# Kernel tuning notes

Hardware: AMD Instinct MI355X
Metric: run time of the kernel (lower is better)

Reference implementation:

```python
import jax, jax.numpy as jnp
import numpy as np

SOS_TOKEN = 0


def setup_inputs() -> dict:
    key = jax.random.key(0)
    ks = jax.random.split(key, 16)
    B, S, T, H, V = 64, 64, 32, 512, 32000
    s = 1.0 / np.sqrt(H)
    inp = {
        "encoder_outputs": jax.random.normal(ks[0], (B, S, H), jnp.float32),
        "encoder_hidden": jax.random.normal(ks[1], (1, B, H), jnp.float32),
        "target_tensor": jax.random.randint(ks[2], (B, T), 0, V),
        "emb": jax.random.normal(ks[3], (V, H), jnp.float32),
        "Wa": jax.random.uniform(ks[4], (H, H), jnp.float32, -s, s),
        "ba": jnp.zeros((H,), jnp.float32),
        "Ua": jax.random.uniform(ks[5], (H, H), jnp.float32, -s, s),
        "bu": jnp.zeros((H,), jnp.float32),
        "va": jax.random.uniform(ks[6], (H, 1), jnp.float32, -s, s),
        "bv": jnp.zeros((1,), jnp.float32),
        "w_ih": jax.random.uniform(ks[7], (3 * H, 2 * H), jnp.float32, -s, s),
        "b_ih": jax.random.uniform(ks[8], (3 * H,), jnp.float32, -s, s),
        "w_hh": jax.random.uniform(ks[9], (3 * H, H), jnp.float32, -s, s),
        "b_hh": jax.random.uniform(ks[10], (3 * H,), jnp.float32, -s, s),
        "Wo": jax.random.uniform(ks[11], (V, H), jnp.float32, -s, s),
        "bo": jax.random.uniform(ks[12], (V,), jnp.float32, -s, s),
    }
    return inp


def _gru_cell(x, h, w_ih, b_ih, w_hh, b_hh):
    # x: [B, 2H], h: [B, H] -- PyTorch nn.GRU gate math
    H = h.shape[-1]
    gi = x @ w_ih.T + b_ih            # [B, 3H]
    gh = h @ w_hh.T + b_hh            # [B, 3H]
    i_r, i_z, i_n = gi[:, :H], gi[:, H:2 * H], gi[:, 2 * H:]
    h_r, h_z, h_n = gh[:, :H], gh[:, H:2 * H], gh[:, 2 * H:]
    r = jax.nn.sigmoid(i_r + h_r)
    z = jax.nn.sigmoid(i_z + h_z)
    n = jnp.tanh(i_n + r * h_n)
    return (1.0 - z) * n + z * h


def reference(encoder_outputs, encoder_hidden, target_tensor,
              emb, Wa, ba, Ua, bu, va, bv,
              w_ih, b_ih, w_hh, b_hh, Wo, bo):
    B, S, H = encoder_outputs.shape
    T = target_tensor.shape[1]
    # Teacher forcing: step t input is SOS for t=0 else target[:, t-1]
    sos = jnp.full((B, 1), SOS_TOKEN, dtype=target_tensor.dtype)
    input_ids = jnp.concatenate([sos, target_tensor[:, :-1]], axis=1)  # [B, T]
    embedded = emb[input_ids]  # [B, T, H]  (dropout is identity in eval)

    # Precompute key projection once (invariant across steps)
    Ua_keys = encoder_outputs @ Ua.T + bu  # [B, S, H]

    def step(h, x_emb):
        # Bahdanau additive attention: query = hidden state
        scores = jnp.tanh(h[:, None, :] @ Wa.T + ba + Ua_keys) @ va + bv  # [B, S, 1]
        scores = scores[..., 0]                                           # [B, S]
        attn = jax.nn.softmax(scores, axis=-1)
        context = jnp.einsum('bs,bsh->bh', attn, encoder_outputs)
        x = jnp.concatenate([x_emb, context], axis=-1)                    # [B, 2H]
        h_new = _gru_cell(x, h, w_ih, b_ih, w_hh, b_hh)
        logits = h_new @ Wo.T + bo                                        # [B, V]
        return h_new, (logits, attn)

    h0 = encoder_hidden[0]  # [B, H]
    h_final, (logits_t, attn_t) = jax.lax.scan(step, h0, jnp.swapaxes(embedded, 0, 1))
    logits = jnp.swapaxes(logits_t, 0, 1)        # [B, T, V]
    attentions = jnp.swapaxes(attn_t, 0, 1)      # [B, T, S]
    log_probs = jax.nn.log_softmax(logits, axis=-1)
    decoder_hidden = h_final[None]               # [1, B, H]
    return (log_probs, decoder_hidden, attentions)
```

## Files before the change

### kernel.cpp

```cpp
#include <hip/hip_runtime.h>

typedef unsigned short u16;
typedef __bf16 bf16x8 __attribute__((ext_vector_type(8)));
typedef float f32x4 __attribute__((ext_vector_type(4)));

#define Bsz 64
#define Ssz 64
#define Tsz 32
#define Hsz 512
#define Vsz 32000
#define NCONV 160
#define NTOT 256

static __device__ inline u16 f2bf(float f) {
    union { float f; unsigned u; } v; v.f = f;
    unsigned u = v.u;
    unsigned r = (u + 0x7FFFu + ((u >> 16) & 1u)) >> 16;
    return (u16)r;
}
static __device__ inline float bf2f(u16 v) {
    union { unsigned u; float f; } x; x.u = ((unsigned)v) << 16; return x.f;
}
static __device__ inline float tanh_fast(float x) {
    float e = __expf(2.f * x);
    return 1.f - 2.f / (e + 1.f);
}
static __device__ inline void st_u32(unsigned* p, unsigned v) {
    __hip_atomic_store(p, v, __ATOMIC_RELAXED, __HIP_MEMORY_SCOPE_AGENT);
}
static __device__ inline unsigned ld_u32(const unsigned* p) {
    return __hip_atomic_load(p, __ATOMIC_RELAXED, __HIP_MEMORY_SCOPE_AGENT);
}

#define GLOAD_LDS16(g, l) \
    __builtin_amdgcn_global_load_lds((const __attribute__((address_space(1))) void*)(g), \
                                     (__attribute__((address_space(3))) void*)(l), 16, 0, 0)

__global__ void prep_kernel(const float* __restrict__ enc, const float* __restrict__ Ua,
                            const float* __restrict__ Wa, const float* __restrict__ wih,
                            const float* __restrict__ whh, const float* __restrict__ ehid,
                            u16* __restrict__ encbf, u16* __restrict__ Uabf,
                            u16* __restrict__ Wabf, u16* __restrict__ wihbf,
                            u16* __restrict__ whhbf, u16* __restrict__ h0bf) {
    const int n0 = 2097152, n1 = 262144, n2 = 262144, n3 = 1572864, n4 = 786432, n5 = 32768;
    const int total = n0 + n1 + n2 + n3 + n4 + n5;
    for (int i = blockIdx.x * blockDim.x + threadIdx.x; i < total; i += gridDim.x * blockDim.x) {
        int j = i;
        if (j < n0) { encbf[j] = f2bf(enc[j]); continue; } j -= n0;
        if (j < n1) { Uabf[j] = f2bf(Ua[j]); continue; } j -= n1;
        if (j < n2) { Wabf[j] = f2bf(Wa[j]); continue; } j -= n2;
        if (j < n3) { wihbf[j] = f2bf(wih[j]); continue; } j -= n3;
        if (j < n4) { whhbf[j] = f2bf(whh[j]); continue; } j -= n4;
        h0bf[j] = f2bf(ehid[j]);
    }
}

__global__ void embed_kernel(const int* __restrict__ target, const float* __restrict__ emb,
                             u16* __restrict__ xbuf) {
    int n = Tsz * Bsz * Hsz;
    for (int i = blockIdx.x * blockDim.x + threadIdx.x; i < n; i += gridDim.x * blockDim.x) {
        int t = i / (Bsz * Hsz);
        int rem = i % (Bsz * Hsz);
        int b = rem / Hsz, k = rem % Hsz;
        int id = (t == 0) ? 0 : target[b * Tsz + (t - 1)];
        xbuf[((size_t)t * Bsz + b) * 1024 + k] = f2bf(emb[(size_t)id * Hsz + k]);
    }
}

__global__ __launch_bounds__(256) void gemm_bt(const u16* __restrict__ A, const u16* __restrict__ Bw,
                                               const float* __restrict__ bias, float* __restrict__ out,
                                               int M, int N, int K) {
    __shared__ __align__(16) u16 As[128 * 32];
    __shared__ __align__(16) u16 Bs[128 * 32];
    int m0 = blockIdx.x * 128, n0 = blockIdx.y * 128;
    int tid = threadIdx.x, lane = tid & 63, wid = tid >> 6;
    int wm = wid & 1, wn = wid >> 1;
    f32x4 acc[4][4] = {};
    for (int k0 = 0; k0 < K; k0 += 32) {
        int e0 = wid * 64 + lane;
        int e1 = e0 + 256;
        GLOAD_LDS16(&A[(size_t)(m0 + (e0 >> 2)) * K + k0 + (e0 & 3) * 8], (char*)As + wid * 1024);
        GLOAD_LDS16(&A[(size_t)(m0 + (e1 >> 2)) * K + k0 + (e1 & 3) * 8], (char*)As + 4096 + wid * 1024);
        GLOAD_LDS16(&Bw[(size_t)(n0 + (e0 >> 2)) * K + k0 + (e0 & 3) * 8], (char*)Bs + wid * 1024);
        GLOAD_LDS16(&Bw[(size_t)(n0 + (e1 >> 2)) * K + k0 + (e1 & 3) * 8], (char*)Bs + 4096 + wid * 1024);
        __syncthreads();
        bf16x8 av[4], bvv[4];
        for (int mi = 0; mi < 4; ++mi)
            av[mi] = *(const bf16x8*)&As[(wm * 64 + mi * 16 + (lane & 15)) * 32 + (lane >> 4) * 8];
        for (int ni = 0; ni < 4; ++ni)
            bvv[ni] = *(const bf16x8*)&Bs[(wn * 64 + ni * 16 + (lane & 15)) * 32 + (lane >> 4) * 8];
        for (int mi = 0; mi < 4; ++mi)
            for (int ni = 0; ni < 4; ++ni)
                acc[mi][ni] = __builtin_amdgcn_mfma_f32_16x16x32_bf16(av[mi], bvv[ni], acc[mi][ni], 0, 0, 0);
        __syncthreads();
    }
    for (int mi = 0; mi < 4; ++mi)
        for (int ni = 0; ni < 4; ++ni) {
            int n = n0 + wn * 64 + ni * 16 + (lane & 15);
            float bb = bias[n];
            for (int r = 0; r < 4; ++r) {
                int m = m0 + wm * 64 + mi * 16 + (lane >> 4) * 4 + r;
                out[(size_t)m * N + n] = acc[mi][ni][r] + bb;
            }
        }
}

static __device__ inline void arrive(unsigned* bar, int slot, unsigned val, int tid) {
    asm volatile("s_waitcnt vmcnt(0)" ::: "memory");
    __syncthreads();
    if (tid == 0) st_u32(&bar[slot * 32], val);
}
static __device__ inline void pollflags(unsigned* bar, int base, int n, unsigned target, int tid) {
    if (tid < n) {
        unsigned* p = &bar[(base + tid) * 32];
        while (ld_u32(p) < target) {}
    }
    __syncthreads();
}

__global__ __launch_bounds__(512, 1) void coop_kernel(
    const float* __restrict__ uak,
    u16* __restrict__ xbuf, u16* __restrict__ Abf,
    const u16* __restrict__ h0bf, const u16* __restrict__ wihbf, const u16* __restrict__ whhbf,
    const u16* __restrict__ Wabf, const float* __restrict__ enc,
    const float* __restrict__ va, const float* __restrict__ bv, const float* __restrict__ ba,
    const float* __restrict__ b_ih, const float* __restrict__ b_hh,
    const float* __restrict__ ehid,
    const float* __restrict__ Wo, u16* __restrict__ Wobf,
    float* __restrict__ out, u16* __restrict__ partials,
    unsigned* __restrict__ bar) {
    __shared__ __align__(16) char lds[149504];
    __shared__ float WhL[512];
    __shared__ float scL[64];
    __shared__ float vaL[512];

    const size_t HID_OFF = (size_t)Bsz * Tsz * Vsz;
    const size_t ATT_OFF = HID_OFF + (size_t)Bsz * Hsz;

    int tid = threadIdx.x, lane = tid & 63, wid = tid >> 6;
    int ln15 = lane & 15, hi = lane >> 4;
    int bx = blockIdx.x;

    unsigned* xbufU = (unsigned*)xbuf;
    unsigned* AbfU = (unsigned*)Abf;
    unsigned* partU = (unsigned*)partials;

    if (bx < 64) {
        int b = bx;
        u16* uakL = (u16*)lds;
        u16* encL = (u16*)(lds + 65536);
        for (int i = tid; i < Ssz * Hsz; i += 512) {
            uakL[i] = f2bf(uak[(size_t)b * Ssz * Hsz + i]);
            encL[i] = f2bf(enc[(size_t)b * Ssz * Hsz + i]);
        }
        vaL[tid] = va[tid];
        float bvv = bv[0];
        float ba_t = ba[tid];
        int halfsel = tid & 1;
        __syncthreads();

        for (int t = 0; t < Tsz; ++t) {
            pollflags(bar, 64, 32, (unsigned)(t + 1), tid);
            {
                float acc = ba_t;
                const unsigned* pb = partU + (size_t)b * 256 + (tid >> 1);
#pragma unroll
                for (int g = 0; g < 32; ++g) {
                    unsigned pw = ld_u32(pb + (size_t)g * 16384);
                    acc += bf2f((u16)(halfsel ? (pw >> 16) : (pw & 0xffff)));
                }
                WhL[tid] = acc;
            }
            __syncthreads();
            for (int si = 0; si < 8; ++si) {
                int s = wid * 8 + si;
                float a = 0.f;
#pragma unroll
                for (int ji = 0; ji < 8; ++ji) {
                    int j = lane + ji * 64;
                    float x = WhL[j] + bf2f(uakL[s * 512 + j]);
                    a += tanh_fast(x) * vaL[j];
                }
                for (int off = 32; off; off >>= 1) a += __shfl_down(a, off);
                if (lane == 0) scL[s] = a + bvv;
            }
            __syncthreads();
            if (wid == 0) {
                float x = scL[lane];
                float mx = x;
                for (int off = 32; off; off >>= 1) mx = fmaxf(mx, __shfl_xor(mx, off));
                float e = __expf(x - mx);
                float sm = e;
                for (int off = 32; off; off >>= 1) sm += __shfl_xor(sm, off);
                float at = e / sm;
                scL[lane] = at;
                out[ATT_OFF + ((size_t)b * Tsz + t) * Ssz + lane] = at;
            }
            __syncthreads();
            float c = 0.f;
            for (int s = 0; s < Ssz; ++s)
                c += scL[s] * bf2f(encL[s * 512 + tid]);
            unsigned me = (unsigned)f2bf(c);
            unsigned other = __shfl_xor(me, 1);
            if ((tid & 1) == 0)
                st_u32(&xbufU[((size_t)t * Bsz + b) * 512 + 256 + (tid >> 1)], me | (other << 16));
            arrive(bar, bx, (unsigned)(t + 1), tid);
        }
    } else if (bx < 96) {
        int g = bx - 64, jbase = g * 16;
        u16* hsl = (u16*)(lds + 147456);
        for (int i = tid; i < 6144; i += 512) {
            int row = i >> 7, c16 = i & 127;
            int Rg = (row >> 4) * 512 + jbase + (row & 15);
            uint4 v = *(const uint4*)&wihbf[(size_t)Rg * 1024 + c16 * 8];
            *(uint4*)(lds + row * 2048 + ((c16 * 16) ^ ((row & 7) << 4))) = v;
        }
        for (int i = tid; i < 3072; i += 512) {
            int row = i >> 6, c16 = i & 63;
            int Rg = (row >> 4) * 512 + jbase + (row & 15);
            uint4 v = *(const uint4*)&whhbf[(size_t)Rg * 512 + c16 * 8];
            *(uint4*)(lds + 98304 + row * 1024 + ((c16 * 16) ^ ((row & 7) << 4))) = v;
        }
        const char* wih_l = lds;
        const char* whh_l = lds + 98304;
        int j = jbase + ln15;
        float bir = b_ih[j] + b_hh[j];
        float biz = b_ih[512 + j] + b_hh[512 + j];
        float bin = b_ih[1024 + j];
        float bhn = b_hh[1024 + j];
        float hp0 = 0.f, hp1 = 0.f, hp2 = 0.f, hp3 = 0.f;
        if (wid < 4) {
            int m = wid;
            hp0 = ehid[(size_t)(m * 16 + hi * 4 + 0) * Hsz + j];
            hp1 = ehid[(size_t)(m * 16 + hi * 4 + 1) * Hsz + j];
            hp2 = ehid[(size_t)(m * 16 + hi * 4 + 2) * Hsz + j];
            hp3 = ehid[(size_t)(m * 16 + hi * 4 + 3) * Hsz + j];
        }
        int swz = (ln15 & 7) << 4;
        bf16x8 zfr = {};
        bf16x8 wfrag[4];
#pragma unroll
        for (int i = 0; i < 4; ++i) {
            int jp = (wid * 4 + i) * 16 + ln15;
            wfrag[i] = (hi < 2) ? *(const bf16x8*)&Wabf[(size_t)jp * 512 + jbase + hi * 8] : zfr;
        }
        for (int i = tid; i < 1024; i += 512)
            hsl[i] = h0bf[(size_t)(i >> 4) * 512 + jbase + (i & 15)];
        __syncthreads();
#pragma unroll
        for (int mt = 0; mt < 4; ++mt) {
            bf16x8 af = (hi < 2) ? *(const bf16x8*)&hsl[(mt * 16 + ln15) * 16 + hi * 8] : zfr;
#pragma unroll
            for (int i = 0; i < 4; ++i) {
                f32x4 pacc = {};
                pacc = __builtin_amdgcn_mfma_f32_16x16x32_bf16(af, wfrag[i], pacc, 0, 0, 0);
                int n0 = (wid * 4 + i) * 16;
#pragma unroll
                for (int r = 0; r < 4; ++r) {
                    int b = mt * 16 + hi * 4 + r;
                    unsigned me = (unsigned)f2bf(pacc[r]);
                    unsigned other = __shfl_xor(me, 1);
                    if ((ln15 & 1) == 0)
                        st_u32(&partU[((size_t)g * 64 + b) * 256 + ((n0 + ln15) >> 1)], me | (other << 16));
                }
            }
        }
        arrive(bar, bx, 1u, tid);

        for (int t = 0; t < Tsz; ++t) {
            const u16* hbt = t ? (Abf + (size_t)(t - 1) * Bsz * Hsz) : h0bf;
            pollflags(bar, 64, 32, (unsigned)(t + 1), tid);
            f32x4 ar = {}, az = {}, ain = {}, ahn = {};
            if (wid < 4) {
                int m = wid;
#pragma unroll 8
                for (int k0 = 0; k0 < 16; ++k0) {
                    bf16x8 a = *(const bf16x8*)&xbuf[((size_t)t * Bsz + m * 16 + ln15) * 1024 + k0 * 32 + hi * 8];
                    int byteIn = k0 * 64 + hi * 16;
                    bf16x8 b0 = *(const bf16x8*)(wih_l + (0 + ln15) * 2048 + (byteIn ^ swz));
                    bf16x8 b1 = *(const bf16x8*)(wih_l + (16 + ln15) * 2048 + (byteIn ^ swz));
                    bf16x8 b2 = *(const bf16x8*)(wih_l + (32 + ln15) * 2048 + (byteIn ^ swz));
                    ar = __builtin_amdgcn_mfma_f32_16x16x32_bf16(a, b0, ar, 0, 0, 0);
                    az = __builtin_amdgcn_mfma_f32_16x16x32_bf16(a, b1, az, 0, 0, 0);
                    ain = __builtin_amdgcn_mfma_f32_16x16x32_bf16(a, b2, ain, 0, 0, 0);
                }
#pragma unroll 8
                for (int k0 = 0; k0 < 16; ++k0) {
                    bf16x8 a = *(const bf16x8*)&hbt[(size_t)(m * 16 + ln15) * 512 + k0 * 32 + hi * 8];
                    int byteIn = k0 * 64 + hi * 16;
                    bf16x8 b0 = *(const bf16x8*)(whh_l + (0 + ln15) * 1024 + (byteIn ^ swz));
                    bf16x8 b1 = *(const bf16x8*)(whh_l + (16 + ln15) * 1024 + (byteIn ^ swz));
                    bf16x8 b2 = *(const bf16x8*)(whh_l + (32 + ln15) * 1024 + (byteIn ^ swz));
                    ar = __builtin_amdgcn_mfma_f32_16x16x32_bf16(a, b0, ar, 0, 0, 0);
                    az = __builtin_amdgcn_mfma_f32_16x16x32_bf16(a, b1, az, 0, 0, 0);
                    ahn = __builtin_amdgcn_mfma_f32_16x16x32_bf16(a, b2, ahn, 0, 0, 0);
                }
                unsigned* p = &bar[(wid * 16 + ln15) * 32];
                while (ld_u32(p) < (unsigned)(t + 1)) {}
#pragma unroll 8
                for (int k0 = 16; k0 < 32; ++k0) {
                    bf16x8 a = *(const bf16x8*)&xbuf[((size_t)t * Bsz + m * 16 + ln15) * 1024 + k0 * 32 + hi * 8];
                    int byteIn = k0 * 64 + hi * 16;
                    bf16x8 b0 = *(const bf16x8*)(wih_l + (0 + ln15) * 2048 + (byteIn ^ swz));
                    bf16x8 b1 = *(const bf16x8*)(wih_l + (16 + ln15) * 2048 + (byteIn ^ swz));
                    bf16x8 b2 = *(const bf16x8*)(wih_l + (32 + ln15) * 2048 + (byteIn ^ swz));
                    ar = __builtin_amdgcn_mfma_f32_16x16x32_bf16(a, b0, ar, 0, 0, 0);
                    az = __builtin_amdgcn_mfma_f32_16x16x32_bf16(a, b1, az, 0, 0, 0);
                    ain = __builtin_amdgcn_mfma_f32_16x16x32_bf16(a, b2, ain, 0, 0, 0);
                }
                float hpv[4] = {hp0, hp1, hp2, hp3};
#pragma unroll
                for (int r = 0; r < 4; ++r) {
                    int b = m * 16 + hi * 4 + r;
                    float rg = 1.f / (1.f + __expf(-(ar[r] + bir)));
                    float zg = 1.f / (1.f + __expf(-(az[r] + biz)));
                    float ng = tanh_fast(ain[r] + bin + rg * (ahn[r] + bhn));
                    float hv = (1.f - zg) * ng + zg * hpv[r];
                    hpv[r] = hv;
                    u16 hb = f2bf(hv);
                    unsigned me = (unsigned)hb;
                    unsigned other = __shfl_xor(me, 1);
                    if ((ln15 & 1) == 0)
                        st_u32(&AbfU[((size_t)t * Bsz + b) * 256 + (j >> 1)], me | (other << 16));
                    hsl[b * 16 + ln15] = hb;
                    if (t == Tsz - 1) out[HID_OFF + (size_t)b * 512 + j] = hv;
                }
                hp0 = hpv[0]; hp1 = hpv[1]; hp2 = hpv[2]; hp3 = hpv[3];
            }
            __syncthreads();
#pragma unroll
            for (int mt = 0; mt < 4; ++mt) {
                bf16x8 af = (hi < 2) ? *(const bf16x8*)&hsl[(mt * 16 + ln15) * 16 + hi * 8] : zfr;
#pragma unroll
                for (int i = 0; i < 4; ++i) {
                    f32x4 pacc = {};
                    pacc = __builtin_amdgcn_mfma_f32_16x16x32_bf16(af, wfrag[i], pacc, 0, 0, 0);
                    int n0 = (wid * 4 + i) * 16;
#pragma unroll
                    for (int r = 0; r < 4; ++r) {
                        int b = mt * 16 + hi * 4 + r;
                        unsigned me = (unsigned)f2bf(pacc[r]);
                        unsigned other = __shfl_xor(me, 1);
                        if ((ln15 & 1) == 0)
                            st_u32(&partU[((size_t)g * 64 + b) * 256 + ((n0 + ln15) >> 1)], me | (other << 16));
                    }
                }
            }
            arrive(bar, bx, (unsigned)(t + 2), tid);
        }
    } else {
        const float4* W4 = (const float4*)Wo;
        for (int i = (bx - 96) * 512 + tid; i < (Vsz * Hsz) / 4; i += NCONV * 512) {
            float4 v = W4[i];
            ushort4 o;
            o.x = f2bf(v.x); o.y = f2bf(v.y); o.z = f2bf(v.z); o.w = f2bf(v.w);
            *(ushort4*)&Wobf[(size_t)i * 4] = o;
        }
    }
}

static __device__ inline void l_stage(const u16* __restrict__ Abf, const u16* __restrict__ Wobf,
                                      int m0, int n0, int k0, char* As, char* Bs, int wid, int lane) {
    int e0 = wid * 64 + lane;
    int r = e0 >> 2, c8 = (e0 & 3) * 8;
    GLOAD_LDS16(&Abf[(size_t)(m0 + r) * 512 + k0 + c8], As + wid * 1024);
    GLOAD_LDS16(&Wobf[(size_t)(n0 + r) * 512 + k0 + c8], Bs + wid * 1024);
    GLOAD_LDS16(&Wobf[(size_t)(n0 + 128 + r) * 512 + k0 + c8], Bs + 8192 + wid * 1024);
}

__global__ __launch_bounds__(512) void gemm_logits(const u16* __restrict__ Abf, const u16* __restrict__ Wobf,
                                                   const float* __restrict__ bo, float* __restrict__ out,
                                                   float* __restrict__ sumexp) {
    __shared__ __align__(16) char lds[49152];
    char* As0 = lds;
    char* Bs0 = lds + 8192;
    char* As1 = lds + 24576;
    char* Bs1 = lds + 32768;
    int tid = threadIdx.x, lane = tid & 63, wid = tid >> 6;
    int ln15 = lane & 15, hi = lane >> 4;
    int wm = wid & 1, wn = wid >> 1;
    int job = blockIdx.x;
    int m0 = (job / 125) * 128, n0 = (job % 125) * 256;
    f32x4 acc[4][4] = {};
    l_stage(Abf, Wobf, m0, n0, 0, As0, Bs0, wid, lane);
#pragma unroll 2
    for (int ks = 0; ks < 16; ++ks) {
        const u16* As = (const u16*)((ks & 1) ? As1 : As0);
        const u16* Bs = (const u16*)((ks & 1) ? Bs1 : Bs0);
        if (ks < 15) {
            l_stage(Abf, Wobf, m0, n0, (ks + 1) * 32,
                    (ks & 1) ? As0 : As1, (ks & 1) ? Bs0 : Bs1, wid, lane);
            asm volatile("s_waitcnt vmcnt(3)" ::: "memory");
        } else {
            asm volatile("s_waitcnt vmcnt(0)" ::: "memory");
        }
        __builtin_amdgcn_s_barrier();
        bf16x8 av[4], bvv[4];
        for (int mi = 0; mi < 4; ++mi)
            av[mi] = *(const bf16x8*)&As[(wm * 64 + mi * 16 + ln15) * 32 + hi * 8];
        for (int ni = 0; ni < 4; ++ni)
            bvv[ni] = *(const bf16x8*)&Bs[(wn * 64 + ni * 16 + ln15) * 32 + hi * 8];
        for (int mi = 0; mi < 4; ++mi)
            for (int ni = 0; ni < 4; ++ni)
                acc[mi][ni] = __builtin_amdgcn_mfma_f32_16x16x32_bf16(av[mi], bvv[ni], acc[mi][ni], 0, 0, 0);
        asm volatile("s_waitcnt lgkmcnt(0)" ::: "memory");
        __builtin_amdgcn_s_barrier();
    }
    float rowpart[4][4];
    for (int mi = 0; mi < 4; ++mi)
        for (int r = 0; r < 4; ++r) rowpart[mi][r] = 0.f;
    for (int mi = 0; mi < 4; ++mi)
        for (int ni = 0; ni < 4; ++ni) {
            int n = n0 + wn * 64 + ni * 16 + ln15;
            float bb = bo[n];
            for (int r = 0; r < 4; ++r) {
                int m = m0 + wm * 64 + mi * 16 + hi * 4 + r;
                int t = m >> 6, b = m & 63;
                float val = acc[mi][ni][r] + bb;
                out[((size_t)(b * Tsz + t)) * Vsz + n] = val;
                rowpart[mi][r] += __expf(val);
            }
        }
    for (int mi = 0; mi < 4; ++mi)
        for (int r = 0; r < 4; ++r) {
            float v = rowpart[mi][r];
            v += __shfl_xor(v, 1);
            v += __shfl_xor(v, 2);
            v += __shfl_xor(v, 4);
            v += __shfl_xor(v, 8);
            if (ln15 == 0) {
                int m = m0 + wm * 64 + mi * 16 + hi * 4 + r;
                atomicAdd(&sumexp[(m & 63) * Tsz + (m >> 6)], v);
            }
        }
}

__global__ void sub_kernel(float* __restrict__ out, const float* __restrict__ sumexp) {
    const int total4 = (Bsz * Tsz * Vsz) / 4;
    float4* o4 = (float4*)out;
    for (int i = blockIdx.x * blockDim.x + threadIdx.x; i < total4; i += gridDim.x * blockDim.x) {
        float l = __logf(sumexp[i / (Vsz / 4)]);
        float4 v = o4[i];
        v.x -= l; v.y -= l; v.z -= l; v.w -= l;
        o4[i] = v;
    }
}

extern "C" void kernel_launch(void* const* d_in, const int* in_sizes, int n_in,
                              void* d_out, int out_size, void* d_ws, size_t ws_size,
                              hipStream_t stream) {
    const float* enc   = (const float*)d_in[0];
    const float* ehid  = (const float*)d_in[1];
    const int*   target= (const int*)d_in[2];
    const float* emb   = (const float*)d_in[3];
    const float* Wa    = (const float*)d_in[4];
    const float* ba    = (const float*)d_in[5];
    const float* Ua    = (const float*)d_in[6];
    const float* bu    = (const float*)d_in[7];
    const float* va    = (const float*)d_in[8];
    const float* bv    = (const float*)d_in[9];
    const float* w_ih  = (const float*)d_in[10];
    const float* b_ih  = (const float*)d_in[11];
    const float* w_hh  = (const float*)d_in[12];
    const float* b_hh  = (const float*)d_in[13];
    const float* Wo    = (const float*)d_in[14];
    const float* bo    = (const float*)d_in[15];
    float* out = (float*)d_out;

    char* w = (char*)d_ws;
    float* uak    = (float*)w; w += (size_t)4096 * 512 * 4;
    float* sumexp = (float*)w; w += 8192;
    unsigned* bar = (unsigned*)w; w += 96 * 128;
    u16* xbuf     = (u16*)w;   w += (size_t)Tsz * Bsz * 1024 * 2;
    u16* Abf      = (u16*)w;   w += (size_t)Tsz * Bsz * Hsz * 2;
    u16* h0bf     = (u16*)w;   w += (size_t)Bsz * Hsz * 2;
    u16* partials = (u16*)w;   w += (size_t)32 * Bsz * Hsz * 2;
    u16* Wabf     = (u16*)w;   w += (size_t)Hsz * Hsz * 2;
    u16* encbf    = (u16*)w;   w += (size_t)4096 * 512 * 2;
    u16* Uabf     = (u16*)w;   w += (size_t)Hsz * Hsz * 2;
    u16* wihbf    = (u16*)w;   w += (size_t)1536 * 1024 * 2;
    u16* whhbf    = (u16*)w;   w += (size_t)1536 * 512 * 2;
    u16* Wobf     = (u16*)w;   w += (size_t)Vsz * 512 * 2;

    prep_kernel<<<2048, 256, 0, stream>>>(enc, Ua, Wa, w_ih, w_hh, ehid,
                                          encbf, Uabf, Wabf, wihbf, whhbf, h0bf);
    embed_kernel<<<1024, 256, 0, stream>>>(target, emb, xbuf);

    gemm_bt<<<dim3(32, 4), 256, 0, stream>>>(encbf, Uabf, bu, uak, 4096, 512, 512);

    hipMemsetAsync(bar, 0, 96 * 128, stream);
    hipMemsetAsync(sumexp, 0, 2048 * 4, stream);

    coop_kernel<<<NTOT, 512, 0, stream>>>(uak, xbuf, Abf, h0bf, wihbf, whhbf,
                                          Wabf, enc, va, bv, ba, b_ih, b_hh,
                                          ehid, Wo, Wobf, out, partials, bar);

    gemm_logits<<<2000, 512, 0, stream>>>(Abf, Wobf, bo, out, sumexp);

    sub_kernel<<<2048, 256, 0, stream>>>(out, sumexp);
}
```

Measured before the change: 976.4 us.

## Fuse logits GEMM into persistent coop kernel, overlapping with recurrent steps

The 160 spare blocks of the persistent kernel, which used to only convert Wo to bf16, now also compute the vocabulary-projection GEMM tiles. Each tile waits on the GRU step flags for the two timesteps it covers, so the logits GEMM runs while later recurrent steps are still executing, and the separate gemm_logits launch is removed. The spin-wait loops also gain s_sleep so polling blocks take fewer issue slots. The costs are extra flag polling, a grid-wide wait on the conversion counter, and competition for memory bandwidth and CUs with the latency-critical recurrent blocks.

```diff
diff --git a/kernel.cpp b/kernel.cpp
--- a/kernel.cpp
+++ b/kernel.cpp
@@ -9,7 +9,7 @@
 #define Tsz 32
 #define Hsz 512
 #define Vsz 32000
-#define NCONV 160
+#define NLBLK 160
 #define NTOT 256
 
 static __device__ inline u16 f2bf(float f) {
@@ -110,10 +110,17 @@
     __syncthreads();
     if (tid == 0) st_u32(&bar[slot * 32], val);
 }
-static __device__ inline void pollflags(unsigned* bar, int base, int n, unsigned target, int tid) {
+static __device__ inline void pollflags1(unsigned* bar, int base, int n, unsigned target, int tid) {
     if (tid < n) {
         unsigned* p = &bar[(base + tid) * 32];
-        while (ld_u32(p) < target) {}
+        while (ld_u32(p) < target) asm volatile("s_sleep 1");
+    }
+    __syncthreads();
+}
+static __device__ inline void pollflags8(unsigned* bar, int base, int n, unsigned target, int tid) {
+    if (tid < n) {
+        unsigned* p = &bar[(base + tid) * 32];
+        while (ld_u32(p) < target) asm volatile("s_sleep 8");
     }
     __syncthreads();
 }
@@ -126,8 +133,8 @@
     const float* __restrict__ va, const float* __restrict__ bv, const float* __restrict__ ba,
     const float* __restrict__ b_ih, const float* __restrict__ b_hh,
     const float* __restrict__ ehid,
-    const float* __restrict__ Wo, u16* __restrict__ Wobf,
-    float* __restrict__ out, u16* __restrict__ partials,
+    const float* __restrict__ Wo, u16* __restrict__ Wobf, const float* __restrict__ bo,
+    float* __restrict__ out, u16* __restrict__ partials, float* __restrict__ sumexp,
     unsigned* __restrict__ bar) {
     __shared__ __align__(16) char lds[149504];
     __shared__ float WhL[512];
@@ -160,7 +167,7 @@
         __syncthreads();
 
         for (int t = 0; t < Tsz; ++t) {
-            pollflags(bar, 64, 32, (unsigned)(t + 1), tid);
+            pollflags1(bar, 64, 32, (unsigned)(t + 1), tid);
             {
                 float acc = ba_t;
                 const unsigned* pb = partU + (size_t)b * 256 + (tid >> 1);
@@ -269,7 +276,7 @@
 
         for (int t = 0; t < Tsz; ++t) {
             const u16* hbt = t ? (Abf + (size_t)(t - 1) * Bsz * Hsz) : h0bf;
-            pollflags(bar, 64, 32, (unsigned)(t + 1), tid);
+            pollflags1(bar, 64, 32, (unsigned)(t + 1), tid);
             f32x4 ar = {}, az = {}, ain = {}, ahn = {};
             if (wid < 4) {
                 int m = wid;
@@ -296,7 +303,7 @@
                     ahn = __builtin_amdgcn_mfma_f32_16x16x32_bf16(a, b2, ahn, 0, 0, 0);
                 }
                 unsigned* p = &bar[(wid * 16 + ln15) * 32];
-                while (ld_u32(p) < (unsigned)(t + 1)) {}
+                while (ld_u32(p) < (unsigned)(t + 1)) asm volatile("s_sleep 1");
 #pragma unroll 8
                 for (int k0 = 16; k0 < 32; ++k0) {
                     bf16x8 a = *(const bf16x8*)&xbuf[((size_t)t * Bsz + m * 16 + ln15) * 1024 + k0 * 32 + hi * 8];
@@ -349,90 +356,100 @@
             arrive(bar, bx, (unsigned)(t + 2), tid);
         }
     } else {
-        const float4* W4 = (const float4*)Wo;
-        for (int i = (bx - 96) * 512 + tid; i < (Vsz * Hsz) / 4; i += NCONV * 512) {
-            float4 v = W4[i];
-            ushort4 o;
-            o.x = f2bf(v.x); o.y = f2bf(v.y); o.z = f2bf(v.z); o.w = f2bf(v.w);
-            *(ushort4*)&Wobf[(size_t)i * 4] = o;
-        }
-    }
-}
-
-static __device__ inline void l_stage(const u16* __restrict__ Abf, const u16* __restrict__ Wobf,
-                                      int m0, int n0, int k0, char* As, char* Bs, int wid, int lane) {
-    int e0 = wid * 64 + lane;
-    int r = e0 >> 2, c8 = (e0 & 3) * 8;
-    GLOAD_LDS16(&Abf[(size_t)(m0 + r) * 512 + k0 + c8], As + wid * 1024);
-    GLOAD_LDS16(&Wobf[(size_t)(n0 + r) * 512 + k0 + c8], Bs + wid * 1024);
-    GLOAD_LDS16(&Wobf[(size_t)(n0 + 128 + r) * 512 + k0 + c8], Bs + 8192 + wid * 1024);
-}
-
-__global__ __launch_bounds__(512) void gemm_logits(const u16* __restrict__ Abf, const u16* __restrict__ Wobf,
-                                                   const float* __restrict__ bo, float* __restrict__ out,
-                                                   float* __restrict__ sumexp) {
-    __shared__ __align__(16) char lds[49152];
-    char* As0 = lds;
-    char* Bs0 = lds + 8192;
-    char* As1 = lds + 24576;
-    char* Bs1 = lds + 32768;
-    int tid = threadIdx.x, lane = tid & 63, wid = tid >> 6;
-    int ln15 = lane & 15, hi = lane >> 4;
-    int wm = wid & 1, wn = wid >> 1;
-    int job = blockIdx.x;
-    int m0 = (job / 125) * 128, n0 = (job % 125) * 256;
-    f32x4 acc[4][4] = {};
-    l_stage(Abf, Wobf, m0, n0, 0, As0, Bs0, wid, lane);
+        unsigned* convdone = &bar[96 * 32];
+        unsigned* WobfU = (unsigned*)Wobf;
+        {
+            const float4* W4 = (const float4*)Wo;
+            for (int i = (bx - 96) * 512 + tid; i < (Vsz * Hsz) / 4; i += NLBLK * 512) {
+                float4 v = W4[i];
+                st_u32(&WobfU[2 * i], (unsigned)f2bf(v.x) | ((unsigned)f2bf(v.y) << 16));
+                st_u32(&WobfU[2 * i + 1], (unsigned)f2bf(v.z) | ((unsigned)f2bf(v.w) << 16));
+            }
+            asm volatile("s_waitcnt vmcnt(0)" ::: "memory");
+            __syncthreads();
+            if (tid == 0) {
+                __hip_atomic_fetch_add(convdone, 1u, __ATOMIC_RELAXED, __HIP_MEMORY_SCOPE_AGENT);
+                while (ld_u32(convdone) < (unsigned)NLBLK) asm volatile("s_sleep 8");
+            }
+            __syncthreads();
+        }
+        char* As0 = lds;
+        char* Bs0 = lds + 8192;
+        char* As1 = lds + 24576;
+        char* Bs1 = lds + 32768;
+        int wm = wid & 1, wn = wid >> 1;
+        int polled_mt = -1;
+        for (int job = bx - 96; job < 2000; job += NLBLK) {
+            int mt = job / 125, nt = job % 125;
+            if (mt != polled_mt) {
+                pollflags8(bar, 64, 32, (unsigned)(2 * mt + 3), tid);
+                polled_mt = mt;
+            }
+            int m0 = mt * 128, n0 = nt * 256;
+            f32x4 acc[4][4] = {};
+            {
+                int e0 = wid * 64 + lane, r = e0 >> 2, c8 = (e0 & 3) * 8;
+                GLOAD_LDS16(&Abf[(size_t)(m0 + r) * 512 + c8], As0 + wid * 1024);
+                GLOAD_LDS16(&Wobf[(size_t)(n0 + r) * 512 + c8], Bs0 + wid * 1024);
+                GLOAD_LDS16(&Wobf[(size_t)(n0 + 128 + r) * 512 + c8], Bs0 + 8192 + wid * 1024);
+            }
 #pragma unroll 2
-    for (int ks = 0; ks < 16; ++ks) {
-        const u16* As = (const u16*)((ks & 1) ? As1 : As0);
-        const u16* Bs = (const u16*)((ks & 1) ? Bs1 : Bs0);
-        if (ks < 15) {
-            l_stage(Abf, Wobf, m0, n0, (ks + 1) * 32,
-                    (ks & 1) ? As0 : As1, (ks & 1) ? Bs0 : Bs1, wid, lane);
-            asm volatile("s_waitcnt vmcnt(3)" ::: "memory");
-        } else {
-            asm volatile("s_waitcnt vmcnt(0)" ::: "memory");
-        }
-        __builtin_amdgcn_s_barrier();
-        bf16x8 av[4], bvv[4];
-        for (int mi = 0; mi < 4; ++mi)
-            av[mi] = *(const bf16x8*)&As[(wm * 64 + mi * 16 + ln15) * 32 + hi * 8];
-        for (int ni = 0; ni < 4; ++ni)
-            bvv[ni] = *(const bf16x8*)&Bs[(wn * 64 + ni * 16 + ln15) * 32 + hi * 8];
-        for (int mi = 0; mi < 4; ++mi)
-            for (int ni = 0; ni < 4; ++ni)
-                acc[mi][ni] = __builtin_amdgcn_mfma_f32_16x16x32_bf16(av[mi], bvv[ni], acc[mi][ni], 0, 0, 0);
-        asm volatile("s_waitcnt lgkmcnt(0)" ::: "memory");
-        __builtin_amdgcn_s_barrier();
-    }
-    float rowpart[4][4];
-    for (int mi = 0; mi < 4; ++mi)
-        for (int r = 0; r < 4; ++r) rowpart[mi][r] = 0.f;
-    for (int mi = 0; mi < 4; ++mi)
-        for (int ni = 0; ni < 4; ++ni) {
-            int n = n0 + wn * 64 + ni * 16 + ln15;
-            float bb = bo[n];
-            for (int r = 0; r < 4; ++r) {
-                int m = m0 + wm * 64 + mi * 16 + hi * 4 + r;
-                int t = m >> 6, b = m & 63;
-                float val = acc[mi][ni][r] + bb;
-                out[((size_t)(b * Tsz + t)) * Vsz + n] = val;
-                rowpart[mi][r] += __expf(val);
-            }
-        }
-    for (int mi = 0; mi < 4; ++mi)
-        for (int r = 0; r < 4; ++r) {
-            float v = rowpart[mi][r];
-            v += __shfl_xor(v, 1);
-            v += __shfl_xor(v, 2);
-            v += __shfl_xor(v, 4);
-            v += __shfl_xor(v, 8);
-            if (ln15 == 0) {
-                int m = m0 + wm * 64 + mi * 16 + hi * 4 + r;
-                atomicAdd(&sumexp[(m & 63) * Tsz + (m >> 6)], v);
-            }
-        }
+            for (int ks = 0; ks < 16; ++ks) {
+                const u16* As = (const u16*)((ks & 1) ? As1 : As0);
+                const u16* Bs = (const u16*)((ks & 1) ? Bs1 : Bs0);
+                if (ks < 15) {
+                    char* Asn = (ks & 1) ? As0 : As1;
+                    char* Bsn = (ks & 1) ? Bs0 : Bs1;
+                    int e0 = wid * 64 + lane, r = e0 >> 2, c8 = (e0 & 3) * 8;
+                    int k0 = (ks + 1) * 32;
+                    GLOAD_LDS16(&Abf[(size_t)(m0 + r) * 512 + k0 + c8], Asn + wid * 1024);
+                    GLOAD_LDS16(&Wobf[(size_t)(n0 + r) * 512 + k0 + c8], Bsn + wid * 1024);
+                    GLOAD_LDS16(&Wobf[(size_t)(n0 + 128 + r) * 512 + k0 + c8], Bsn + 8192 + wid * 1024);
+                    asm volatile("s_waitcnt vmcnt(3)" ::: "memory");
+                } else {
+                    asm volatile("s_waitcnt vmcnt(0)" ::: "memory");
+                }
+                __builtin_amdgcn_s_barrier();
+                bf16x8 av[4], bvv[4];
+                for (int mi = 0; mi < 4; ++mi)
+                    av[mi] = *(const bf16x8*)&As[(wm * 64 + mi * 16 + ln15) * 32 + hi * 8];
+                for (int ni = 0; ni < 4; ++ni)
+                    bvv[ni] = *(const bf16x8*)&Bs[(wn * 64 + ni * 16 + ln15) * 32 + hi * 8];
+                for (int mi = 0; mi < 4; ++mi)
+                    for (int ni = 0; ni < 4; ++ni)
+                        acc[mi][ni] = __builtin_amdgcn_mfma_f32_16x16x32_bf16(av[mi], bvv[ni], acc[mi][ni], 0, 0, 0);
+                asm volatile("s_waitcnt lgkmcnt(0)" ::: "memory");
+                __builtin_amdgcn_s_barrier();
+            }
+            float rowpart[4][4];
+            for (int mi = 0; mi < 4; ++mi)
+                for (int r = 0; r < 4; ++r) rowpart[mi][r] = 0.f;
+            for (int mi = 0; mi < 4; ++mi)
+                for (int ni = 0; ni < 4; ++ni) {
+                    int n = n0 + wn * 64 + ni * 16 + ln15;
+                    float bb = bo[n];
+                    for (int r = 0; r < 4; ++r) {
+                        int m = m0 + wm * 64 + mi * 16 + hi * 4 + r;
+                        int t = m >> 6, b = m & 63;
+                        float val = acc[mi][ni][r] + bb;
+                        out[((size_t)(b * Tsz + t)) * Vsz + n] = val;
+                        rowpart[mi][r] += __expf(val);
+                    }
+                }
+            for (int mi = 0; mi < 4; ++mi)
+                for (int r = 0; r < 4; ++r) {
+                    float v = rowpart[mi][r];
+                    v += __shfl_xor(v, 1);
+                    v += __shfl_xor(v, 2);
+                    v += __shfl_xor(v, 4);
+                    v += __shfl_xor(v, 8);
+                    if (ln15 == 0) {
+                        int m = m0 + wm * 64 + mi * 16 + hi * 4 + r;
+                        atomicAdd(&sumexp[(m & 63) * Tsz + (m >> 6)], v);
+                    }
+                }
+        }
+    }
 }
 
 __global__ void sub_kernel(float* __restrict__ out, const float* __restrict__ sumexp) {
@@ -470,7 +487,7 @@
     char* w = (char*)d_ws;
     float* uak    = (float*)w; w += (size_t)4096 * 512 * 4;
     float* sumexp = (float*)w; w += 8192;
-    unsigned* bar = (unsigned*)w; w += 96 * 128;
+    unsigned* bar = (unsigned*)w; w += 128 * 128;
     u16* xbuf     = (u16*)w;   w += (size_t)Tsz * Bsz * 1024 * 2;
     u16* Abf      = (u16*)w;   w += (size_t)Tsz * Bsz * Hsz * 2;
     u16* h0bf     = (u16*)w;   w += (size_t)Bsz * Hsz * 2;
@@ -488,14 +505,12 @@
 
     gemm_bt<<<dim3(32, 4), 256, 0, stream>>>(encbf, Uabf, bu, uak, 4096, 512, 512);
 
-    hipMemsetAsync(bar, 0, 96 * 128, stream);
+    hipMemsetAsync(bar, 0, 128 * 128, stream);
     hipMemsetAsync(sumexp, 0, 2048 * 4, stream);
 
     coop_kernel<<<NTOT, 512, 0, stream>>>(uak, xbuf, Abf, h0bf, wihbf, whhbf,
                                           Wabf, enc, va, bv, ba, b_ih, b_hh,
-                                          ehid, Wo, Wobf, out, partials, bar);
-
-    gemm_logits<<<2000, 512, 0, stream>>>(Abf, Wobf, bo, out, sumexp);
+                                          ehid, Wo, Wobf, bo, out, partials, sumexp, bar);
 
     sub_kernel<<<2048, 256, 0, stream>>>(out, sumexp);
 }
```

Measured after the change: 986.3 us. About the same (+1.0%).
